# Performance work log

Measured on AMD Instinct MI355X. Metric: run time of the kernel, lower is better.

The kernel has to match this reference:

```python
import jax, jax.numpy as jnp
import numpy as np

EPS = 1e-6
SMOOTH = 0.025


def setup_inputs() -> dict:
    key = jax.random.key(0)
    k1, = jax.random.split(key, 1)
    x = jax.random.uniform(k1, (32, 128, 8000), dtype=jnp.float32)  # (B, C, T) energies >= 0
    alpha = jnp.float32(0.98)
    delta = jnp.float32(2.0)
    r = jnp.float32(0.5)
    return {"x": x, "alpha": alpha, "delta": delta, "r": r}


def reference(x, alpha, delta, r):
    # x: (B, C, T)
    x = jnp.maximum(x, 0.0)
    xt = jnp.moveaxis(x, -1, 0)  # (T, B, C) for time scan

    def ema_step(M, xt_t):
        M = (1.0 - SMOOTH) * M + SMOOTH * xt_t
        return M, M

    M0 = jnp.zeros(x.shape[:2], dtype=x.dtype)  # (B, C)
    _, Mt = jax.lax.scan(ema_step, M0, xt)  # (T, B, C)
    M = jnp.moveaxis(Mt, 0, -1)  # (B, C, T)

    norm = x / jnp.power(EPS + M, alpha)
    y = jnp.power(norm + delta, r) - jnp.power(delta, r)
    return y
```

## Files before the change

kernel.cpp:

```cpp
#include <hip/hip_runtime.h>

#define EPSV   1e-6f
#define SMOOTH 0.025f

__device__ __forceinline__ float fast_log2(float v) { return __builtin_amdgcn_logf(v); }
__device__ __forceinline__ float fast_exp2(float v) { return __builtin_amdgcn_exp2f(v); }

__device__ __forceinline__ float pcen_elem(float xr, float M, float alpha,
                                           float delta, float r, float dr) {
    float m    = EPSV + M;
    float norm = xr * fast_exp2(-alpha * fast_log2(m));
    return fast_exp2(r * fast_log2(norm + delta)) - dr;
}

__global__ __launch_bounds__(256) void pcen_ema_kernel(
    const float* __restrict__ x,
    const float* __restrict__ alpha_p,
    const float* __restrict__ delta_p,
    const float* __restrict__ r_p,
    float* __restrict__ y,
    int rows, int T)
{
    const int gid  = blockIdx.x * blockDim.x + threadIdx.x;
    const int row  = gid >> 6;
    const int lane = gid & 63;
    if (row >= rows) return;

    const float alpha = alpha_p[0];
    const float delta = delta_p[0];
    const float r     = r_p[0];
    const float dr    = fast_exp2(r * fast_log2(delta));

    const float a  = 1.0f - SMOOTH;
    const float b  = SMOOTH;
    const float a2 = a  * a;
    const float a3 = a2 * a;
    const float a4 = a2 * a2;
    const float c0 = a4;
    const float c1 = c0 * c0;
    const float c2 = c1 * c1;
    const float c3 = c2 * c2;
    const float c4 = c3 * c3;
    const float c5 = c4 * c4;

    float a4lane = 1.0f;
    if (lane & 1)  a4lane *= c0;
    if (lane & 2)  a4lane *= c1;
    if (lane & 4)  a4lane *= c2;
    if (lane & 8)  a4lane *= c3;
    if (lane & 16) a4lane *= c4;
    if (lane & 32) a4lane *= c5;
    float alane = 1.0f;
    if (lane & 1)  alane *= a;
    if (lane & 2)  alane *= a2;
    if (lane & 4)  alane *= a4;
    if (lane & 8)  alane *= c1;
    if (lane & 16) alane *= c2;
    if (lane & 32) alane *= c3;

    const long long base = (long long)row * T;
    const float4* __restrict__ xin  = (const float4*)(x + base);
    float4* __restrict__       yout = (float4*)(y + base);

    float m0 = 0.0f;
    const int ntiles = T >> 8;

    for (int tile = 0; tile < ntiles; ++tile) {
        float4 xv = xin[tile * 64 + lane];
        float x1 = fmaxf(xv.x, 0.0f), x2 = fmaxf(xv.y, 0.0f);
        float x3 = fmaxf(xv.z, 0.0f), x4 = fmaxf(xv.w, 0.0f);

        float q1 = b * x1;
        float q2 = fmaf(a, q1, b * x2);
        float q3 = fmaf(a, q2, b * x3);
        float q4 = fmaf(a, q3, b * x4);

        float P = q4, up;
        up = __shfl_up(P, 1, 64);  P = fmaf(lane >= 1  ? c0 : 0.0f, up, P);
        up = __shfl_up(P, 2, 64);  P = fmaf(lane >= 2  ? c1 : 0.0f, up, P);
        up = __shfl_up(P, 4, 64);  P = fmaf(lane >= 4  ? c2 : 0.0f, up, P);
        up = __shfl_up(P, 8, 64);  P = fmaf(lane >= 8  ? c3 : 0.0f, up, P);
        up = __shfl_up(P, 16, 64); P = fmaf(lane >= 16 ? c4 : 0.0f, up, P);
        up = __shfl_up(P, 32, 64); P = fmaf(lane >= 32 ? c5 : 0.0f, up, P);
        float Pexc = __shfl_up(P, 1, 64);
        if (lane == 0) Pexc = 0.0f;

        float state = fmaf(a4lane, m0, Pexc);
        float M1 = fmaf(a,  state, q1);
        float M2 = fmaf(a2, state, q2);
        float M3 = fmaf(a3, state, q3);
        float M4 = fmaf(a4, state, q4);
        m0 = __shfl(M4, 63, 64);

        float4 yv;
        yv.x = pcen_elem(x1, M1, alpha, delta, r, dr);
        yv.y = pcen_elem(x2, M2, alpha, delta, r, dr);
        yv.z = pcen_elem(x3, M3, alpha, delta, r, dr);
        yv.w = pcen_elem(x4, M4, alpha, delta, r, dr);
        yout[tile * 64 + lane] = yv;
    }

    const int t0  = ntiles << 8;
    const int rem = T - t0;
    if (rem > 0) {
        const bool act = lane < rem;
        float xr = act ? fmaxf(x[base + t0 + lane], 0.0f) : 0.0f;
        float q = b * xr;
        float P = q, up;
        up = __shfl_up(P, 1, 64);  P = fmaf(lane >= 1  ? a  : 0.0f, up, P);
        up = __shfl_up(P, 2, 64);  P = fmaf(lane >= 2  ? a2 : 0.0f, up, P);
        up = __shfl_up(P, 4, 64);  P = fmaf(lane >= 4  ? a4 : 0.0f, up, P);
        up = __shfl_up(P, 8, 64);  P = fmaf(lane >= 8  ? c1 : 0.0f, up, P);
        up = __shfl_up(P, 16, 64); P = fmaf(lane >= 16 ? c2 : 0.0f, up, P);
        up = __shfl_up(P, 32, 64); P = fmaf(lane >= 32 ? c3 : 0.0f, up, P);
        float Pexc = __shfl_up(P, 1, 64);
        if (lane == 0) Pexc = 0.0f;
        float state = fmaf(alane, m0, Pexc);
        float M = fmaf(a, state, q);
        if (act) y[base + t0 + lane] = pcen_elem(xr, M, alpha, delta, r, dr);
    }
}

extern "C" void kernel_launch(void* const* d_in, const int* in_sizes, int n_in,
                              void* d_out, int out_size, void* d_ws, size_t ws_size,
                              hipStream_t stream) {
    const float* x     = (const float*)d_in[0];
    const float* alpha = (const float*)d_in[1];
    const float* delta = (const float*)d_in[2];
    const float* r     = (const float*)d_in[3];
    float* y = (float*)d_out;

    const int T     = 8000;
    const int total = in_sizes[0];
    const int rows  = total / T;

    const int threads = rows * 64;
    const int block   = 256;
    const int grid    = (threads + block - 1) / block;
    pcen_ema_kernel<<<grid, block, 0, stream>>>(x, alpha, delta, r, y, rows, T);
}
```

Measured before the change: 58.37 us.

## Split each row's EMA scan across two waves with warm-up approximation

```diff
diff --git a/kernel.cpp b/kernel.cpp
--- a/kernel.cpp
+++ b/kernel.cpp
@@ -2,18 +2,61 @@
 
 #define EPSV   1e-6f
 #define SMOOTH 0.025f
+#define HALF   4096
+#define WARM   512
 
 __device__ __forceinline__ float fast_log2(float v) { return __builtin_amdgcn_logf(v); }
 __device__ __forceinline__ float fast_exp2(float v) { return __builtin_amdgcn_exp2f(v); }
 
-__device__ __forceinline__ float pcen_elem(float xr, float M, float alpha,
+__device__ __forceinline__ float pcen_elem(float xr, float M, float nalpha,
                                            float delta, float r, float dr) {
     float m    = EPSV + M;
-    float norm = xr * fast_exp2(-alpha * fast_log2(m));
+    float norm = xr * fast_exp2(nalpha * fast_log2(m));
     return fast_exp2(r * fast_log2(norm + delta)) - dr;
 }
 
-__global__ __launch_bounds__(256) void pcen_ema_kernel(
+struct C8 {
+    float a1,a2,a3,a4,a5,a6,a7,a8;
+    float d0,d1,d2,d3,d4,d5;
+    float a8lane;
+    float b;
+    int   lane;
+};
+
+__device__ __forceinline__ float scan8(const C8& c, const float xr[8],
+                                       float m0, float M[8]) {
+    float q0 = c.b * xr[0];
+    float q1 = fmaf(c.a1, q0, c.b * xr[1]);
+    float q2 = fmaf(c.a1, q1, c.b * xr[2]);
+    float q3 = fmaf(c.a1, q2, c.b * xr[3]);
+    float q4 = fmaf(c.a1, q3, c.b * xr[4]);
+    float q5 = fmaf(c.a1, q4, c.b * xr[5]);
+    float q6 = fmaf(c.a1, q5, c.b * xr[6]);
+    float q7 = fmaf(c.a1, q6, c.b * xr[7]);
+
+    float P = q7, up;
+    up = __shfl_up(P, 1, 64);  P = fmaf(c.lane >= 1  ? c.d0 : 0.0f, up, P);
+    up = __shfl_up(P, 2, 64);  P = fmaf(c.lane >= 2  ? c.d1 : 0.0f, up, P);
+    up = __shfl_up(P, 4, 64);  P = fmaf(c.lane >= 4  ? c.d2 : 0.0f, up, P);
+    up = __shfl_up(P, 8, 64);  P = fmaf(c.lane >= 8  ? c.d3 : 0.0f, up, P);
+    up = __shfl_up(P, 16, 64); P = fmaf(c.lane >= 16 ? c.d4 : 0.0f, up, P);
+    up = __shfl_up(P, 32, 64); P = fmaf(c.lane >= 32 ? c.d5 : 0.0f, up, P);
+    float Pexc = __shfl_up(P, 1, 64);
+    if (c.lane == 0) Pexc = 0.0f;
+
+    float state = fmaf(c.a8lane, m0, Pexc);
+    M[0] = fmaf(c.a1, state, q0);
+    M[1] = fmaf(c.a2, state, q1);
+    M[2] = fmaf(c.a3, state, q2);
+    M[3] = fmaf(c.a4, state, q3);
+    M[4] = fmaf(c.a5, state, q4);
+    M[5] = fmaf(c.a6, state, q5);
+    M[6] = fmaf(c.a7, state, q6);
+    M[7] = fmaf(c.a8, state, q7);
+    return __shfl(M[7], 63, 64);
+}
+
+__global__ __launch_bounds__(256, 8) void pcen_ema_kernel(
     const float* __restrict__ x,
     const float* __restrict__ alpha_p,
     const float* __restrict__ delta_p,
@@ -21,103 +64,105 @@
     float* __restrict__ y,
     int rows, int T)
 {
-    const int gid  = blockIdx.x * blockDim.x + threadIdx.x;
-    const int row  = gid >> 6;
-    const int lane = gid & 63;
+    const int gid   = blockIdx.x * blockDim.x + threadIdx.x;
+    const int wave  = gid >> 6;
+    const int lane  = gid & 63;
+    const int row   = wave >> 1;
+    const int chunk = wave & 1;
     if (row >= rows) return;
 
-    const float alpha = alpha_p[0];
-    const float delta = delta_p[0];
-    const float r     = r_p[0];
-    const float dr    = fast_exp2(r * fast_log2(delta));
+    const float nalpha = -alpha_p[0];
+    const float delta  = delta_p[0];
+    const float r      = r_p[0];
+    const float dr     = fast_exp2(r * fast_log2(delta));
 
-    const float a  = 1.0f - SMOOTH;
-    const float b  = SMOOTH;
-    const float a2 = a  * a;
-    const float a3 = a2 * a;
-    const float a4 = a2 * a2;
-    const float c0 = a4;
-    const float c1 = c0 * c0;
-    const float c2 = c1 * c1;
-    const float c3 = c2 * c2;
-    const float c4 = c3 * c3;
-    const float c5 = c4 * c4;
-
-    float a4lane = 1.0f;
-    if (lane & 1)  a4lane *= c0;
-    if (lane & 2)  a4lane *= c1;
-    if (lane & 4)  a4lane *= c2;
-    if (lane & 8)  a4lane *= c3;
-    if (lane & 16) a4lane *= c4;
-    if (lane & 32) a4lane *= c5;
-    float alane = 1.0f;
-    if (lane & 1)  alane *= a;
-    if (lane & 2)  alane *= a2;
-    if (lane & 4)  alane *= a4;
-    if (lane & 8)  alane *= c1;
-    if (lane & 16) alane *= c2;
-    if (lane & 32) alane *= c3;
+    C8 c;
+    c.lane = lane;
+    c.b  = SMOOTH;
+    const float a = 1.0f - SMOOTH;
+    c.a1 = a;        c.a2 = a*a;      c.a3 = c.a2*a;   c.a4 = c.a2*c.a2;
+    c.a5 = c.a4*a;   c.a6 = c.a4*c.a2; c.a7 = c.a4*c.a3; c.a8 = c.a4*c.a4;
+    c.d0 = c.a8;       c.d1 = c.d0*c.d0; c.d2 = c.d1*c.d1;
+    c.d3 = c.d2*c.d2;  c.d4 = c.d3*c.d3; c.d5 = c.d4*c.d4;
+    float a8l = 1.0f;
+    if (lane & 1)  a8l *= c.d0;
+    if (lane & 2)  a8l *= c.d1;
+    if (lane & 4)  a8l *= c.d2;
+    if (lane & 8)  a8l *= c.d3;
+    if (lane & 16) a8l *= c.d4;
+    if (lane & 32) a8l *= c.d5;
+    c.a8lane = a8l;
 
     const long long base = (long long)row * T;
-    const float4* __restrict__ xin  = (const float4*)(x + base);
-    float4* __restrict__       yout = (float4*)(y + base);
+    const float* __restrict__ xrow = x + base;
+    float* __restrict__       yrow = y + base;
+
+    const int tstart = chunk ? HALF : 0;
+    const int tend   = chunk ? T    : HALF;
 
     float m0 = 0.0f;
-    const int ntiles = T >> 8;
 
-    for (int tile = 0; tile < ntiles; ++tile) {
-        float4 xv = xin[tile * 64 + lane];
-        float x1 = fmaxf(xv.x, 0.0f), x2 = fmaxf(xv.y, 0.0f);
-        float x3 = fmaxf(xv.z, 0.0f), x4 = fmaxf(xv.w, 0.0f);
-
-        float q1 = b * x1;
-        float q2 = fmaf(a, q1, b * x2);
-        float q3 = fmaf(a, q2, b * x3);
-        float q4 = fmaf(a, q3, b * x4);
-
-        float P = q4, up;
-        up = __shfl_up(P, 1, 64);  P = fmaf(lane >= 1  ? c0 : 0.0f, up, P);
-        up = __shfl_up(P, 2, 64);  P = fmaf(lane >= 2  ? c1 : 0.0f, up, P);
-        up = __shfl_up(P, 4, 64);  P = fmaf(lane >= 4  ? c2 : 0.0f, up, P);
-        up = __shfl_up(P, 8, 64);  P = fmaf(lane >= 8  ? c3 : 0.0f, up, P);
-        up = __shfl_up(P, 16, 64); P = fmaf(lane >= 16 ? c4 : 0.0f, up, P);
-        up = __shfl_up(P, 32, 64); P = fmaf(lane >= 32 ? c5 : 0.0f, up, P);
-        float Pexc = __shfl_up(P, 1, 64);
-        if (lane == 0) Pexc = 0.0f;
-
-        float state = fmaf(a4lane, m0, Pexc);
-        float M1 = fmaf(a,  state, q1);
-        float M2 = fmaf(a2, state, q2);
-        float M3 = fmaf(a3, state, q3);
-        float M4 = fmaf(a4, state, q4);
-        m0 = __shfl(M4, 63, 64);
-
-        float4 yv;
-        yv.x = pcen_elem(x1, M1, alpha, delta, r, dr);
-        yv.y = pcen_elem(x2, M2, alpha, delta, r, dr);
-        yv.z = pcen_elem(x3, M3, alpha, delta, r, dr);
-        yv.w = pcen_elem(x4, M4, alpha, delta, r, dr);
-        yout[tile * 64 + lane] = yv;
+    if (chunk) {
+        const int tw = HALF - WARM;
+        float4 w0 = *(const float4*)(xrow + tw + 8 * lane);
+        float4 w1 = *(const float4*)(xrow + tw + 8 * lane + 4);
+        float xr[8] = { fmaxf(w0.x,0.f), fmaxf(w0.y,0.f), fmaxf(w0.z,0.f), fmaxf(w0.w,0.f),
+                        fmaxf(w1.x,0.f), fmaxf(w1.y,0.f), fmaxf(w1.z,0.f), fmaxf(w1.w,0.f) };
+        float Mt[8];
+        m0 = scan8(c, xr, 0.0f, Mt);
     }
 
-    const int t0  = ntiles << 8;
-    const int rem = T - t0;
-    if (rem > 0) {
-        const bool act = lane < rem;
-        float xr = act ? fmaxf(x[base + t0 + lane], 0.0f) : 0.0f;
-        float q = b * xr;
-        float P = q, up;
-        up = __shfl_up(P, 1, 64);  P = fmaf(lane >= 1  ? a  : 0.0f, up, P);
-        up = __shfl_up(P, 2, 64);  P = fmaf(lane >= 2  ? a2 : 0.0f, up, P);
-        up = __shfl_up(P, 4, 64);  P = fmaf(lane >= 4  ? a4 : 0.0f, up, P);
-        up = __shfl_up(P, 8, 64);  P = fmaf(lane >= 8  ? c1 : 0.0f, up, P);
-        up = __shfl_up(P, 16, 64); P = fmaf(lane >= 16 ? c2 : 0.0f, up, P);
-        up = __shfl_up(P, 32, 64); P = fmaf(lane >= 32 ? c3 : 0.0f, up, P);
-        float Pexc = __shfl_up(P, 1, 64);
-        if (lane == 0) Pexc = 0.0f;
-        float state = fmaf(alane, m0, Pexc);
-        float M = fmaf(a, state, q);
-        if (act) y[base + t0 + lane] = pcen_elem(xr, M, alpha, delta, r, dr);
+    const int nfull = (tend - tstart) >> 9;
+    int t = tstart;
+
+    float4 v0 = make_float4(0,0,0,0), v1 = v0;
+    if (nfull > 0) {
+        v0 = *(const float4*)(xrow + t + 8 * lane);
+        v1 = *(const float4*)(xrow + t + 8 * lane + 4);
+    }
+    for (int i = 0; i < nfull; ++i) {
+        float4 n0 = make_float4(0,0,0,0), n1 = n0;
+        const int tn = t + 512;
+        if (i + 1 < nfull) {
+            n0 = *(const float4*)(xrow + tn + 8 * lane);
+            n1 = *(const float4*)(xrow + tn + 8 * lane + 4);
+        }
+
+        float xr[8] = { fmaxf(v0.x,0.f), fmaxf(v0.y,0.f), fmaxf(v0.z,0.f), fmaxf(v0.w,0.f),
+                        fmaxf(v1.x,0.f), fmaxf(v1.y,0.f), fmaxf(v1.z,0.f), fmaxf(v1.w,0.f) };
+        float M[8];
+        m0 = scan8(c, xr, m0, M);
+
+        float4 o0, o1;
+        o0.x = pcen_elem(xr[0], M[0], nalpha, delta, r, dr);
+        o0.y = pcen_elem(xr[1], M[1], nalpha, delta, r, dr);
+        o0.z = pcen_elem(xr[2], M[2], nalpha, delta, r, dr);
+        o0.w = pcen_elem(xr[3], M[3], nalpha, delta, r, dr);
+        o1.x = pcen_elem(xr[4], M[4], nalpha, delta, r, dr);
+        o1.y = pcen_elem(xr[5], M[5], nalpha, delta, r, dr);
+        o1.z = pcen_elem(xr[6], M[6], nalpha, delta, r, dr);
+        o1.w = pcen_elem(xr[7], M[7], nalpha, delta, r, dr);
+        *(float4*)(yrow + t + 8 * lane)     = o0;
+        *(float4*)(yrow + t + 8 * lane + 4) = o1;
+
+        v0 = n0; v1 = n1; t = tn;
+    }
+
+    if (t < tend) {
+        const int b8 = t + 8 * lane;
+        float xr[8];
+        #pragma unroll
+        for (int k = 0; k < 8; ++k) {
+            int idx = b8 + k;
+            xr[k] = (idx < tend) ? fmaxf(xrow[idx], 0.0f) : 0.0f;
+        }
+        float M[8];
+        scan8(c, xr, m0, M);
+        #pragma unroll
+        for (int k = 0; k < 8; ++k) {
+            int idx = b8 + k;
+            if (idx < tend) yrow[idx] = pcen_elem(xr[k], M[k], nalpha, delta, r, dr);
+        }
     }
 }
 
@@ -134,7 +179,8 @@
     const int total = in_sizes[0];
     const int rows  = total / T;
 
-    const int threads = rows * 64;
+    const int waves   = rows * 2;
+    const int threads = waves * 64;
     const int block   = 256;
     const int grid    = (threads + block - 1) / block;
     pcen_ema_kernel<<<grid, block, 0, stream>>>(x, alpha, delta, r, y, rows, T);
```

After: 62.83 us. 7.6% more time.
